# Optimization experiments

Measured on AMD Instinct MI355X. Metric: run time of the kernel, lower is better.

Reference implementation:

```python
import jax, jax.numpy as jnp
import numpy as np

N = 100000   # nodes
E = 1600000  # edges
D_IN = 7
H1 = 64
H2 = 32
G = 64       # graphs in batch


def setup_inputs() -> dict:
    key = jax.random.key(0)
    ks = jax.random.split(key, 10)
    x = jax.random.normal(ks[0], (N, D_IN), jnp.float32)
    edge_index = jax.random.randint(ks[1], (2, E), 0, N, dtype=jnp.int64)
    batch = jnp.sort(jax.random.randint(ks[2], (N,), 0, G, dtype=jnp.int64))
    # Glorot-style init for GCN weights
    W1 = jax.random.normal(ks[3], (D_IN, H1), jnp.float32) * (1.0 / np.sqrt(D_IN))
    b1 = jnp.zeros((H1,), jnp.float32)
    W2 = jax.random.normal(ks[4], (H1, H2), jnp.float32) * (1.0 / np.sqrt(H1))
    b2 = jnp.zeros((H2,), jnp.float32)
    W3 = jax.random.normal(ks[5], (H1, H2), jnp.float32) * (1.0 / np.sqrt(H1))
    b3 = jnp.zeros((H2,), jnp.float32)
    eps = jax.random.normal(ks[6], (N, H2), jnp.float32)  # reparam noise
    return dict(x=x, edge_index=edge_index, batch=batch,
                W1=W1, b1=b1, W2=W2, b2=b2, W3=W3, b3=b3, eps=eps)


def _gcn_agg(xw, src, dst, dis):
    # Symmetric-normalized aggregation with self-loops (PyG GCNConv default):
    # out[i] = sum_{(j->i)} d_i^{-1/2} d_j^{-1/2} xw[j] + d_i^{-1} xw[i]
    norm = (dis[src] * dis[dst])[:, None]
    msg = xw[src] * norm                      # [E, H] gather
    out = jax.ops.segment_sum(msg, dst, num_segments=N)  # scatter-add
    return out + xw * (dis * dis)[:, None]    # self-loop term


def reference(x, edge_index, batch, W1, b1, W2, b2, W3, b3, eps):
    src, dst = edge_index[0], edge_index[1]
    # degree on A + I (targets), unit edge weights
    deg = jax.ops.segment_sum(jnp.ones((E,), x.dtype), dst, num_segments=N) + 1.0
    dis = jax.lax.rsqrt(deg)  # deg^{-1/2}

    hidden1 = jax.nn.relu(_gcn_agg(x @ W1, src, dst, dis) + b1)

    # global mean pool of raw x over graphs
    counts = jax.ops.segment_sum(jnp.ones((N,), x.dtype), batch, num_segments=G)
    x_pooled = jax.ops.segment_sum(x, batch, num_segments=G) / jnp.maximum(counts, 1.0)[:, None]

    mu = jax.nn.relu(_gcn_agg(hidden1 @ W2, src, dst, dis) + b2)
    logvar = jax.nn.relu(_gcn_agg(hidden1 @ W3, src, dst, dis) + b3)

    # reparameterize: std = exp(logvar) (no 0.5 factor, as in source)
    z = eps * jnp.exp(logvar) + mu
    return z, x_pooled, mu, logvar
```

## Files before the change

### kernel.cpp

```cpp
#include <hip/hip_runtime.h>
#include <hip/hip_bf16.h>
#include <hip/hip_fp16.h>

#define NN 100000
#define NE 1600000
#define D_IN 7
#define H1 64
#define H2 32
#define NG 64
#define TE 2048
#define NTILE 782
#define BSH 9
#define NBUK 196
#define CAP 10240

typedef _Float16 f16x8 __attribute__((ext_vector_type(8)));
typedef float f32x4 __attribute__((ext_vector_type(4)));

__device__ int lower_bound_i(const int* a, int n, int v) {
    int lo = 0, hi = n;
    while (lo < hi) { int mid = (lo + hi) >> 1; if (a[mid] < v) lo = mid + 1; else hi = mid; }
    return lo;
}

__global__ void k_pi(const float* __restrict__ x, const int* __restrict__ batch,
                     float* __restrict__ outp, int* __restrict__ bucket_cursor) {
    int g = blockIdx.x, t = threadIdx.x;
    if (g == NG) {
        if (t < 256) bucket_cursor[t] = t * CAP;
        return;
    }
    __shared__ int bounds[2];
    __shared__ float red[256 * D_IN];
    if (t == 0) {
        bounds[0] = lower_bound_i(batch, NN, g);
        bounds[1] = lower_bound_i(batch, NN, g + 1);
    }
    __syncthreads();
    int s = bounds[0], e = bounds[1];
    float acc[D_IN];
#pragma unroll
    for (int k = 0; k < D_IN; k++) acc[k] = 0.f;
    for (int n = s + t; n < e; n += 256) {
#pragma unroll
        for (int k = 0; k < D_IN; k++) acc[k] += x[n * D_IN + k];
    }
#pragma unroll
    for (int k = 0; k < D_IN; k++) red[t * D_IN + k] = acc[k];
    __syncthreads();
    if (t < D_IN) {
        float sum = 0.f;
        for (int i = 0; i < 256; i++) sum += red[i * D_IN + t];
        float cnt = (float)(e - s);
        outp[g * D_IN + t] = sum / fmaxf(cnt, 1.f);
    }
}

__global__ __launch_bounds__(256) void k_bin(const int* __restrict__ src,
                                             const int* __restrict__ dst,
                                             int* __restrict__ bucket_cursor,
                                             int* __restrict__ staging) {
    __shared__ int hist[NBUK];
    __shared__ int startx[NBUK];
    __shared__ int runb[NBUK];
    __shared__ int cur[NBUK];
    __shared__ int wsum[4];
    __shared__ int2 pairs[TE];
    int t = threadIdx.x;
    int base = blockIdx.x * TE;
    int tile_cnt = min(TE, NE - base);
    for (int i = t; i < NBUK; i += 256) hist[i] = 0;
    __syncthreads();
    int myd[TE / 256], mys[TE / 256];
#pragma unroll
    for (int k = 0; k < TE / 256; k++) {
        int i = base + k * 256 + t;
        if (i < NE) {
            myd[k] = dst[i]; mys[k] = src[i];
            atomicAdd(&hist[myd[k] >> BSH], 1);
        } else myd[k] = -1;
    }
    __syncthreads();
    int hv = (t < NBUK) ? hist[t] : 0;
    int lane = t & 63, wv = t >> 6;
    int sv = hv;
#pragma unroll
    for (int off = 1; off < 64; off <<= 1) {
        int n = __shfl_up(sv, off, 64);
        if (lane >= off) sv += n;
    }
    if (lane == 63) wsum[wv] = sv;
    __syncthreads();
    int wbase = 0;
#pragma unroll
    for (int i = 0; i < 4; i++) wbase += (i < wv) ? wsum[i] : 0;
    if (t < NBUK) {
        int ex = wbase + sv - hv;
        startx[t] = ex;
        cur[t] = ex;
        if (hv > 0) runb[t] = atomicAdd(&bucket_cursor[t], hv);
    }
    __syncthreads();
#pragma unroll
    for (int k = 0; k < TE / 256; k++) {
        if (myd[k] >= 0) {
            int b = myd[k] >> BSH;
            int slot = atomicAdd(&cur[b], 1);
            pairs[slot] = make_int2(myd[k], mys[k]);
        }
    }
    __syncthreads();
    for (int i = t; i < tile_cnt; i += 256) {
        int2 p = pairs[i];
        int b = p.x >> BSH;
        staging[runb[b] + (i - startx[b])] = ((p.x & 511) << 17) | p.y;
    }
}

__global__ __launch_bounds__(512) void k_build(const int* __restrict__ staging,
                                               const int* __restrict__ bucket_cursor,
                                               int2* __restrict__ rowinfo,
                                               float* __restrict__ dis,
                                               int* __restrict__ csr,
                                               const float* __restrict__ x,
                                               float* __restrict__ xd8) {
    __shared__ int cnt[512];
    __shared__ int cur[512];
    __shared__ int wsum[8];
    int t = threadIdx.x;
    int nbase = blockIdx.x << BSH;
    int ebase = blockIdx.x * CAP;
    int eend = bucket_cursor[blockIdx.x];
    cnt[t] = 0;
    __syncthreads();
    for (int i = ebase + t; i < eend; i += 512)
        atomicAdd(&cnt[staging[i] >> 17], 1);
    __syncthreads();
    int v = cnt[t];
    int lane = t & 63, wv = t >> 6;
    int sv = v;
#pragma unroll
    for (int off = 1; off < 64; off <<= 1) {
        int n = __shfl_up(sv, off, 64);
        if (lane >= off) sv += n;
    }
    if (lane == 63) wsum[wv] = sv;
    __syncthreads();
    int wbase = 0;
#pragma unroll
    for (int i = 0; i < 8; i++) wbase += (i < wv) ? wsum[i] : 0;
    int excl = wbase + sv - v;
    cur[t] = excl;
    int node = nbase + t;
    if (node < NN) {
        rowinfo[node] = make_int2(ebase + excl, v);
        float d = rsqrtf((float)v + 1.0f);
        dis[node] = d;
        const float* xr = x + (size_t)node * D_IN;
        float4 w0 = make_float4(d * xr[0], d * xr[1], d * xr[2], d * xr[3]);
        float4 w1 = make_float4(d * xr[4], d * xr[5], d * xr[6], 0.f);
        float4* xo = (float4*)(xd8 + (size_t)node * 8);
        xo[0] = w0; xo[1] = w1;
    }
    __syncthreads();
    for (int i = ebase + t; i < eend; i += 512) {
        int p = staging[i];
        int pos = ebase + atomicAdd(&cur[p >> 17], 1);
        csr[pos] = p & 0x1FFFF;
    }
}

__global__ __launch_bounds__(256) void k_aggx(const int2* __restrict__ rowinfo,
                                              const float* __restrict__ dis,
                                              const int* __restrict__ csr,
                                              const float* __restrict__ xd8,
                                              const float* __restrict__ W1,
                                              const float* __restrict__ b1,
                                              __half* __restrict__ h1h) {
    __shared__ float sW[D_IN * H1];
    __shared__ float sb[H1];
    __shared__ float sAx[64 * 9];
    int t = threadIdx.x;
    for (int i = t; i < D_IN * H1; i += 256) sW[i] = W1[i];
    if (t < H1) sb[t] = b1[t];
    int ll = t & 3;
    int ln = t >> 2;
    int node = blockIdx.x * 64 + ln;
    int nodec = min(node, NN - 1);
    int2 ri = rowinfo[nodec];
    int start = ri.x, c = ri.y;
    int cpos = start + max(c - 1, 0);
    int cmax = c;
    cmax = max(cmax, __shfl_xor(cmax, 4, 64));
    cmax = max(cmax, __shfl_xor(cmax, 8, 64));
    cmax = max(cmax, __shfl_xor(cmax, 16, 64));
    cmax = max(cmax, __shfl_xor(cmax, 32, 64));
    const float2* xb = (const float2*)xd8;
    float2 acc[4];
#pragma unroll
    for (int k = 0; k < 4; k++) acc[k] = make_float2(0.f, 0.f);
    for (int j = 0; j < cmax; j += 16) {
        int sarr[16];
#pragma unroll
        for (int k = 0; k < 16; k++) {
            int s = csr[min(start + j + k, cpos)];
            sarr[k] = ((j + k) < c) ? s : nodec;
        }
        float2 r[16];
#pragma unroll
        for (int k = 0; k < 16; k++) r[k] = xb[(size_t)sarr[k] * 4 + ll];
#pragma unroll
        for (int k = 0; k < 16; k++) {
            bool v = (j + k) < c;
            acc[k & 3].x += v ? r[k].x : 0.f;
            acc[k & 3].y += v ? r[k].y : 0.f;
        }
    }
    float sx = acc[0].x + acc[1].x + acc[2].x + acc[3].x;
    float sy = acc[0].y + acc[1].y + acc[2].y + acc[3].y;
    float2 self = xb[(size_t)nodec * 4 + ll];
    float dn = dis[nodec];
    sAx[ln * 9 + 2 * ll]     = dn * (sx + self.x);
    sAx[ln * 9 + 2 * ll + 1] = dn * (sy + self.y);
    __syncthreads();
    if (node < NN) {
        const float* axp = &sAx[ln * 9];
        union { __half h[16]; float4 f[2]; } u;
#pragma unroll
        for (int j = 0; j < 16; j++) {
            int h = ll * 16 + j;
            float a = sb[h];
#pragma unroll
            for (int k = 0; k < D_IN; k++) a += axp[k] * sW[k * H1 + h];
            u.h[j] = __float2half(dn * fmaxf(a, 0.f));
        }
        float4* d4 = (float4*)(h1h + (size_t)node * H1 + ll * 16);
        d4[0] = u.f[0];
        d4[1] = u.f[1];
    }
}

__device__ __forceinline__ void pk_acc4(__half2* a, float4 r, bool v) {
    unsigned u0 = v ? *reinterpret_cast<unsigned*>(&r.x) : 0u;
    unsigned u1 = v ? *reinterpret_cast<unsigned*>(&r.y) : 0u;
    unsigned u2 = v ? *reinterpret_cast<unsigned*>(&r.z) : 0u;
    unsigned u3 = v ? *reinterpret_cast<unsigned*>(&r.w) : 0u;
    a[0] = __hadd2(a[0], *reinterpret_cast<__half2*>(&u0));
    a[1] = __hadd2(a[1], *reinterpret_cast<__half2*>(&u1));
    a[2] = __hadd2(a[2], *reinterpret_cast<__half2*>(&u2));
    a[3] = __hadd2(a[3], *reinterpret_cast<__half2*>(&u3));
}

__global__ __launch_bounds__(256) void k_agg2f(const int2* __restrict__ rowinfo,
                                               const float* __restrict__ dis,
                                               const int* __restrict__ csr,
                                               const __half* __restrict__ h1h,
                                               const float* __restrict__ W2,
                                               const float* __restrict__ W3,
                                               const float* __restrict__ b2,
                                               const float* __restrict__ b3,
                                               const float* __restrict__ eps,
                                               float* __restrict__ out_z,
                                               float* __restrict__ out_mu,
                                               float* __restrict__ out_lv) {
    __shared__ __align__(16) _Float16 sW[64 * 80];
    __shared__ __align__(16) _Float16 sT[64 * 72];
    int t = threadIdx.x;
    for (int i = t; i < 64 * 64; i += 256) {
        int c = i >> 6, k = i & 63;
        float w = (c < 32) ? W2[k * H2 + c] : W3[k * H2 + (c - 32)];
        sW[c * 80 + k] = (_Float16)w;
    }
    int lane = t & 63;
    int wv = t >> 6;
    int l7 = lane & 7, sub8 = lane >> 3;
    const float4* yb4 = (const float4*)h1h;
    for (int g = 0; g < 2; g++) {
        int lrow = wv * 16 + g * 8 + sub8;
        int node = blockIdx.x * 64 + lrow;
        int nodec = min(node, NN - 1);
        int2 ri = rowinfo[nodec];
        int start = ri.x, c = ri.y;
        int cpos = start + max(c - 1, 0);
        int cmax = c;
        cmax = max(cmax, __shfl_xor(cmax, 8, 64));
        cmax = max(cmax, __shfl_xor(cmax, 16, 64));
        cmax = max(cmax, __shfl_xor(cmax, 32, 64));
        __half2 z2 = __float2half2_rn(0.f);
        __half2 acc[4][4];
#pragma unroll
        for (int i = 0; i < 4; i++)
#pragma unroll
            for (int k = 0; k < 4; k++) acc[i][k] = z2;
        for (int j = 0; j < cmax; j += 16) {
            int sarr[16];
#pragma unroll
            for (int k = 0; k < 16; k++) {
                int s = csr[min(start + j + k, cpos)];
                sarr[k] = ((j + k) < c) ? s : nodec;
            }
            float4 r[16];
#pragma unroll
            for (int k = 0; k < 16; k++)
                r[k] = yb4[(size_t)sarr[k] * 8 + l7];
#pragma unroll
            for (int k = 0; k < 16; k++)
                pk_acc4(acc[k & 3], r[k], (j + k) < c);
        }
        __half2 s0 = __hadd2(__hadd2(acc[0][0], acc[1][0]), __hadd2(acc[2][0], acc[3][0]));
        __half2 s1 = __hadd2(__hadd2(acc[0][1], acc[1][1]), __hadd2(acc[2][1], acc[3][1]));
        __half2 s2 = __hadd2(__hadd2(acc[0][2], acc[1][2]), __hadd2(acc[2][2], acc[3][2]));
        __half2 s3 = __hadd2(__hadd2(acc[0][3], acc[1][3]), __hadd2(acc[2][3], acc[3][3]));
        float4 selfv = yb4[(size_t)nodec * 8 + l7];
        __half2* sh = reinterpret_cast<__half2*>(&selfv);
        float dn = dis[nodec];
        float2 f0 = __half22float2(s0), e0 = __half22float2(sh[0]);
        float2 f1 = __half22float2(s1), e1 = __half22float2(sh[1]);
        float2 f2 = __half22float2(s2), e2 = __half22float2(sh[2]);
        float2 f3 = __half22float2(s3), e3 = __half22float2(sh[3]);
        __half2 o0, o1, o2, o3;
        o0.x = __float2half(dn * (f0.x + e0.x)); o0.y = __float2half(dn * (f0.y + e0.y));
        o1.x = __float2half(dn * (f1.x + e1.x)); o1.y = __float2half(dn * (f1.y + e1.y));
        o2.x = __float2half(dn * (f2.x + e2.x)); o2.y = __float2half(dn * (f2.y + e2.y));
        o3.x = __float2half(dn * (f3.x + e3.x)); o3.y = __float2half(dn * (f3.y + e3.y));
        float4 st;
        st.x = *reinterpret_cast<float*>(&o0);
        st.y = *reinterpret_cast<float*>(&o1);
        st.z = *reinterpret_cast<float*>(&o2);
        st.w = *reinterpret_cast<float*>(&o3);
        *(float4*)&sT[lrow * 72 + l7 * 8] = st;
    }
    __syncthreads();
    int sub = lane >> 4, l15 = lane & 15;
    int c15 = l15, k8 = sub;
    const _Float16* ap = &sT[(wv * 16 + c15) * 72];
    f16x8 a0 = *(const f16x8*)(ap + k8 * 8);
    f16x8 a1 = *(const f16x8*)(ap + 32 + k8 * 8);
    const _Float16* wb = sW + (size_t)c15 * 80 + k8 * 8;
    f16x8 b00 = *(const f16x8*)(wb);
    f16x8 b01 = *(const f16x8*)(wb + 32);
    f16x8 b10 = *(const f16x8*)(wb + 16 * 80);
    f16x8 b11 = *(const f16x8*)(wb + 16 * 80 + 32);
    f16x8 b20 = *(const f16x8*)(wb + 32 * 80);
    f16x8 b21 = *(const f16x8*)(wb + 32 * 80 + 32);
    f16x8 b30 = *(const f16x8*)(wb + 48 * 80);
    f16x8 b31 = *(const f16x8*)(wb + 48 * 80 + 32);
    f32x4 ac0 = {0.f, 0.f, 0.f, 0.f};
    f32x4 ac1 = ac0, ac2 = ac0, ac3 = ac0;
    ac0 = __builtin_amdgcn_mfma_f32_16x16x32_f16(a0, b00, ac0, 0, 0, 0);
    ac0 = __builtin_amdgcn_mfma_f32_16x16x32_f16(a1, b01, ac0, 0, 0, 0);
    ac1 = __builtin_amdgcn_mfma_f32_16x16x32_f16(a0, b10, ac1, 0, 0, 0);
    ac1 = __builtin_amdgcn_mfma_f32_16x16x32_f16(a1, b11, ac1, 0, 0, 0);
    ac2 = __builtin_amdgcn_mfma_f32_16x16x32_f16(a0, b20, ac2, 0, 0, 0);
    ac2 = __builtin_amdgcn_mfma_f32_16x16x32_f16(a1, b21, ac2, 0, 0, 0);
    ac3 = __builtin_amdgcn_mfma_f32_16x16x32_f16(a0, b30, ac3, 0, 0, 0);
    ac3 = __builtin_amdgcn_mfma_f32_16x16x32_f16(a1, b31, ac3, 0, 0, 0);
    float bb2a = b2[c15], bb2b = b2[c15 + 16];
    float bb3a = b3[c15], bb3b = b3[c15 + 16];
    int srow = blockIdx.x * 64 + wv * 16 + k8 * 4;
#pragma unroll
    for (int i = 0; i < 4; i++) {
        int r = srow + i;
        if (r < NN) {
            float mu0 = fmaxf(ac0[i] + bb2a, 0.f);
            float mu1 = fmaxf(ac1[i] + bb2b, 0.f);
            float lv0 = fmaxf(ac2[i] + bb3a, 0.f);
            float lv1 = fmaxf(ac3[i] + bb3b, 0.f);
            size_t o0 = (size_t)r * 32 + c15;
            float e0 = eps[o0], e1 = eps[o0 + 16];
            out_mu[o0]      = mu0;
            out_mu[o0 + 16] = mu1;
            out_lv[o0]      = lv0;
            out_lv[o0 + 16] = lv1;
            out_z[o0]       = e0 * __expf(lv0) + mu0;
            out_z[o0 + 16]  = e1 * __expf(lv1) + mu1;
        }
    }
}

extern "C" void kernel_launch(void* const* d_in, const int* in_sizes, int n_in,
                              void* d_out, int out_size, void* d_ws, size_t ws_size,
                              hipStream_t stream) {
    const float* x   = (const float*)d_in[0];
    const int*   ei  = (const int*)d_in[1];
    const int*   bat = (const int*)d_in[2];
    const float* W1  = (const float*)d_in[3];
    const float* b1  = (const float*)d_in[4];
    const float* W2  = (const float*)d_in[5];
    const float* b2  = (const float*)d_in[6];
    const float* W3  = (const float*)d_in[7];
    const float* b3  = (const float*)d_in[8];
    const float* eps = (const float*)d_in[9];

    const int* src = ei;
    const int* dst = ei + NE;

    float* out = (float*)d_out;
    float* out_z    = out;
    float* out_pool = out + (size_t)NN * H2;
    float* out_mu   = out_pool + NG * D_IN;
    float* out_lv   = out_mu + (size_t)NN * H2;

    int*    bucket_cursor = (int*)d_ws;
    int2*   rowinfo       = (int2*)(bucket_cursor + 256);
    float*  dis           = (float*)(rowinfo + NN);
    int*    staging       = (int*)(dis + NN);
    int*    csr           = staging + (size_t)NBUK * CAP;
    __half* h1h           = (__half*)(csr + (size_t)NBUK * CAP);
    float*  xd8           = (float*)(h1h + (size_t)NN * H1);

    k_pi    <<<NG + 1, 256, 0, stream>>>(x, bat, out_pool, bucket_cursor);
    k_bin   <<<NTILE, 256, 0, stream>>>(src, dst, bucket_cursor, staging);
    k_build <<<NBUK, 512, 0, stream>>>(staging, bucket_cursor, rowinfo, dis, csr, x, xd8);
    k_aggx  <<<(NN + 63) / 64, 256, 0, stream>>>(rowinfo, dis, csr, xd8, W1, b1, h1h);
    k_agg2f <<<(NN + 63) / 64, 256, 0, stream>>>(rowinfo, dis, csr, h1h, W2, W3,
                                                 b2, b3, eps, out_z, out_mu, out_lv);
}
```

Measured before the change: 205.4 us.

## Slice hidden features into four column slabs and split aggregation from matmul

The layer-1 output is now stored as four 16-column slabs, each laid out node-major. The layer-2 aggregation runs one slab per block, so each gather touches a 25.6K-row, 3.2MB working set, which improves L2 locality for random neighbour reads. The MFMA projection and epilogue move into a separate kernel that reads the aggregated slabs back from global memory. This adds an extra kernel launch and a round trip of the intermediate through global memory, and each slab re-reads the CSR indices four times.

```diff
diff --git a/kernel.cpp b/kernel.cpp
--- a/kernel.cpp
+++ b/kernel.cpp
@@ -176,7 +176,7 @@
                                               const float* __restrict__ xd8,
                                               const float* __restrict__ W1,
                                               const float* __restrict__ b1,
-                                              __half* __restrict__ h1h) {
+                                              __half* __restrict__ h1s) {
     __shared__ float sW[D_IN * H1];
     __shared__ float sb[H1];
     __shared__ float sAx[64 * 9];
@@ -234,7 +234,7 @@
             for (int k = 0; k < D_IN; k++) a += axp[k] * sW[k * H1 + h];
             u.h[j] = __float2half(dn * fmaxf(a, 0.f));
         }
-        float4* d4 = (float4*)(h1h + (size_t)node * H1 + ll * 16);
+        float4* d4 = (float4*)(h1s + ((size_t)ll * NN + node) * 16);
         d4[0] = u.f[0];
         d4[1] = u.f[1];
     }
@@ -251,38 +251,27 @@
     a[3] = __hadd2(a[3], *reinterpret_cast<__half2*>(&u3));
 }
 
-__global__ __launch_bounds__(256) void k_agg2f(const int2* __restrict__ rowinfo,
+__global__ __launch_bounds__(256) void k_agg2s(const int2* __restrict__ rowinfo,
                                                const float* __restrict__ dis,
                                                const int* __restrict__ csr,
-                                               const __half* __restrict__ h1h,
-                                               const float* __restrict__ W2,
-                                               const float* __restrict__ W3,
-                                               const float* __restrict__ b2,
-                                               const float* __restrict__ b3,
-                                               const float* __restrict__ eps,
-                                               float* __restrict__ out_z,
-                                               float* __restrict__ out_mu,
-                                               float* __restrict__ out_lv) {
-    __shared__ __align__(16) _Float16 sW[64 * 80];
-    __shared__ __align__(16) _Float16 sT[64 * 72];
+                                               const __half* __restrict__ h1s,
+                                               __half* __restrict__ sAgg) {
     int t = threadIdx.x;
-    for (int i = t; i < 64 * 64; i += 256) {
-        int c = i >> 6, k = i & 63;
-        float w = (c < 32) ? W2[k * H2 + c] : W3[k * H2 + (c - 32)];
-        sW[c * 80 + k] = (_Float16)w;
-    }
+    int sl = blockIdx.x & 3;
+    int nb = blockIdx.x >> 2;
     int lane = t & 63;
     int wv = t >> 6;
-    int l7 = lane & 7, sub8 = lane >> 3;
-    const float4* yb4 = (const float4*)h1h;
+    int l1 = lane & 1, sub32 = lane >> 1;
+    const float4* tb = (const float4*)(h1s + (size_t)sl * NN * 16);
     for (int g = 0; g < 2; g++) {
-        int lrow = wv * 16 + g * 8 + sub8;
-        int node = blockIdx.x * 64 + lrow;
+        int node = nb * 256 + wv * 64 + g * 32 + sub32;
         int nodec = min(node, NN - 1);
         int2 ri = rowinfo[nodec];
         int start = ri.x, c = ri.y;
         int cpos = start + max(c - 1, 0);
         int cmax = c;
+        cmax = max(cmax, __shfl_xor(cmax, 2, 64));
+        cmax = max(cmax, __shfl_xor(cmax, 4, 64));
         cmax = max(cmax, __shfl_xor(cmax, 8, 64));
         cmax = max(cmax, __shfl_xor(cmax, 16, 64));
         cmax = max(cmax, __shfl_xor(cmax, 32, 64));
@@ -302,7 +291,7 @@
             float4 r[16];
 #pragma unroll
             for (int k = 0; k < 16; k++)
-                r[k] = yb4[(size_t)sarr[k] * 8 + l7];
+                r[k] = tb[(size_t)sarr[k] * 2 + l1];
 #pragma unroll
             for (int k = 0; k < 16; k++)
                 pk_acc4(acc[k & 3], r[k], (j + k) < c);
@@ -311,7 +300,7 @@
         __half2 s1 = __hadd2(__hadd2(acc[0][1], acc[1][1]), __hadd2(acc[2][1], acc[3][1]));
         __half2 s2 = __hadd2(__hadd2(acc[0][2], acc[1][2]), __hadd2(acc[2][2], acc[3][2]));
         __half2 s3 = __hadd2(__hadd2(acc[0][3], acc[1][3]), __hadd2(acc[2][3], acc[3][3]));
-        float4 selfv = yb4[(size_t)nodec * 8 + l7];
+        float4 selfv = tb[(size_t)nodec * 2 + l1];
         __half2* sh = reinterpret_cast<__half2*>(&selfv);
         float dn = dis[nodec];
         float2 f0 = __half22float2(s0), e0 = __half22float2(sh[0]);
@@ -323,19 +312,44 @@
         o1.x = __float2half(dn * (f1.x + e1.x)); o1.y = __float2half(dn * (f1.y + e1.y));
         o2.x = __float2half(dn * (f2.x + e2.x)); o2.y = __float2half(dn * (f2.y + e2.y));
         o3.x = __float2half(dn * (f3.x + e3.x)); o3.y = __float2half(dn * (f3.y + e3.y));
-        float4 st;
-        st.x = *reinterpret_cast<float*>(&o0);
-        st.y = *reinterpret_cast<float*>(&o1);
-        st.z = *reinterpret_cast<float*>(&o2);
-        st.w = *reinterpret_cast<float*>(&o3);
-        *(float4*)&sT[lrow * 72 + l7 * 8] = st;
-    }
-    __syncthreads();
+        if (node < NN) {
+            float4 st;
+            st.x = *reinterpret_cast<float*>(&o0);
+            st.y = *reinterpret_cast<float*>(&o1);
+            st.z = *reinterpret_cast<float*>(&o2);
+            st.w = *reinterpret_cast<float*>(&o3);
+            ((float4*)(sAgg + ((size_t)sl * NN + node) * 16))[l1] = st;
+        }
+    }
+}
+
+__global__ __launch_bounds__(256) void k_mm23(const __half* __restrict__ sAgg,
+                                              const float* __restrict__ W2,
+                                              const float* __restrict__ W3,
+                                              const float* __restrict__ b2,
+                                              const float* __restrict__ b3,
+                                              const float* __restrict__ eps,
+                                              float* __restrict__ out_z,
+                                              float* __restrict__ out_mu,
+                                              float* __restrict__ out_lv) {
+    __shared__ __align__(16) _Float16 sW[64 * 80];
+    int t = threadIdx.x;
+    for (int i = t; i < 64 * 64; i += 256) {
+        int c = i >> 6, k = i & 63;
+        float w = (c < 32) ? W2[k * H2 + c] : W3[k * H2 + (c - 32)];
+        sW[c * 80 + k] = (_Float16)w;
+    }
+    __syncthreads();
+    int lane = t & 63;
+    int wv = t >> 6;
     int sub = lane >> 4, l15 = lane & 15;
     int c15 = l15, k8 = sub;
-    const _Float16* ap = &sT[(wv * 16 + c15) * 72];
-    f16x8 a0 = *(const f16x8*)(ap + k8 * 8);
-    f16x8 a1 = *(const f16x8*)(ap + 32 + k8 * 8);
+    int r0 = blockIdx.x * 64 + wv * 16;
+    int rowc = min(r0 + c15, NN - 1);
+    int slice0 = k8 >> 1;
+    int off0 = (k8 & 1) * 8;
+    f16x8 a0 = *(const f16x8*)(sAgg + ((size_t)slice0 * NN + rowc) * 16 + off0);
+    f16x8 a1 = *(const f16x8*)(sAgg + ((size_t)(slice0 + 2) * NN + rowc) * 16 + off0);
     const _Float16* wb = sW + (size_t)c15 * 80 + k8 * 8;
     f16x8 b00 = *(const f16x8*)(wb);
     f16x8 b01 = *(const f16x8*)(wb + 32);
@@ -357,7 +371,7 @@
     ac3 = __builtin_amdgcn_mfma_f32_16x16x32_f16(a1, b31, ac3, 0, 0, 0);
     float bb2a = b2[c15], bb2b = b2[c15 + 16];
     float bb3a = b3[c15], bb3b = b3[c15 + 16];
-    int srow = blockIdx.x * 64 + wv * 16 + k8 * 4;
+    int srow = r0 + k8 * 4;
 #pragma unroll
     for (int i = 0; i < 4; i++) {
         int r = srow + i;
@@ -406,13 +420,15 @@
     float*  dis           = (float*)(rowinfo + NN);
     int*    staging       = (int*)(dis + NN);
     int*    csr           = staging + (size_t)NBUK * CAP;
-    __half* h1h           = (__half*)(csr + (size_t)NBUK * CAP);
-    float*  xd8           = (float*)(h1h + (size_t)NN * H1);
+    __half* h1s           = (__half*)(csr + (size_t)NBUK * CAP);
+    float*  xd8           = (float*)(h1s + (size_t)NN * H1);
+    __half* sAgg          = (__half*)(xd8 + (size_t)NN * 8);
 
     k_pi    <<<NG + 1, 256, 0, stream>>>(x, bat, out_pool, bucket_cursor);
     k_bin   <<<NTILE, 256, 0, stream>>>(src, dst, bucket_cursor, staging);
     k_build <<<NBUK, 512, 0, stream>>>(staging, bucket_cursor, rowinfo, dis, csr, x, xd8);
-    k_aggx  <<<(NN + 63) / 64, 256, 0, stream>>>(rowinfo, dis, csr, xd8, W1, b1, h1h);
-    k_agg2f <<<(NN + 63) / 64, 256, 0, stream>>>(rowinfo, dis, csr, h1h, W2, W3,
-                                                 b2, b3, eps, out_z, out_mu, out_lv);
-}
+    k_aggx  <<<(NN + 63) / 64, 256, 0, stream>>>(rowinfo, dis, csr, xd8, W1, b1, h1s);
+    k_agg2s <<<4 * ((NN + 255) / 256), 256, 0, stream>>>(rowinfo, dis, csr, h1s, sAgg);
+    k_mm23  <<<(NN + 63) / 64, 256, 0, stream>>>(sAgg, W2, W3, b2, b3, eps,
+                                                 out_z, out_mu, out_lv);
+}
```

New measurement: 241.1 us. +17.3%, slower.
